# Optimization experiments

Measured on AMD Instinct MI355X. Metric: run time of the kernel, lower is better.

## Reference

```python
import jax, jax.numpy as jnp
import numpy as np
from jax import lax

B, T = 64, 2048
VOCAB, E, H = 50000, 256, 256
PADDING_TOKEN = 0

def setup_inputs() -> dict:
    key = jax.random.key(0)
    ks = jax.random.split(key, 7)
    batch_reviews = jax.random.randint(ks[0], (B, T), 0, VOCAB)
    batch_lengths = jax.random.randint(ks[1], (B,), 1, T + 1)  # valid lengths in [1, T]
    emb_table = jax.random.normal(ks[2], (VOCAB, E), dtype=jnp.float32)
    emb_table = emb_table.at[PADDING_TOKEN].set(0.0)
    s_ih = 1.0 / np.sqrt(H)
    W_ih = jax.random.uniform(ks[3], (H, E), minval=-s_ih, maxval=s_ih, dtype=jnp.float32)
    W_hh = jax.random.uniform(ks[4], (H, H), minval=-s_ih, maxval=s_ih, dtype=jnp.float32)
    s_c = 1.0 / np.sqrt(H)
    W_cls = jax.random.uniform(ks[5], (2, H), minval=-s_c, maxval=s_c, dtype=jnp.float32)
    b_cls = jax.random.uniform(ks[6], (2,), minval=-s_c, maxval=s_c, dtype=jnp.float32)
    return {"batch_reviews": batch_reviews, "batch_lengths": batch_lengths,
            "emb_table": emb_table, "W_ih": W_ih, "W_hh": W_hh,
            "W_cls": W_cls, "b_cls": b_cls}

def reference(batch_reviews, batch_lengths, emb_table, W_ih, W_hh, W_cls, b_cls):
    # padding_idx row contributes zero embedding
    table = emb_table.at[PADDING_TOKEN].set(0.0)
    data = table[batch_reviews]  # [B, T, E]
    # Precompute input projections for all steps in one GEMM: [B, T, H]
    x_proj = jnp.einsum('bte,he->bth', data, W_ih)
    h0 = jnp.zeros((data.shape[0], W_hh.shape[0]), dtype=data.dtype)

    def step(h, xp_t):  # xp_t: [B, H]
        h_new = jnp.tanh(xp_t + h @ W_hh.T)
        return h_new, h_new

    _, hs = lax.scan(step, h0, jnp.swapaxes(x_proj, 0, 1))  # hs: [T, B, H]
    hs = jnp.swapaxes(hs, 0, 1)  # [B, T, H]
    last = hs[jnp.arange(hs.shape[0]), batch_lengths - 1]  # [B, H]
    logits = last @ W_cls.T + b_cls  # [B, 2]
    return logits
```

## Files before the change

### kernel.cpp

```cpp
#include <hip/hip_runtime.h>
#include <hip/hip_bf16.h>

#define VOCAB 50000
#define EDIM 256
#define HDIM 256
#define BATCH 64
#define SEQ 2048

__global__ void k_transpose(const float* __restrict__ W, float* __restrict__ WT) {
    int idx = blockIdx.x * 256 + threadIdx.x;
    int e = idx >> 8;
    int i = idx & 255;
    WT[idx] = W[i * 256 + e];
}

__global__ __launch_bounds__(256) void k_project(const float* __restrict__ emb,
                                                 const float* __restrict__ WT,
                                                 float* __restrict__ P) {
    __shared__ float etile[32 * 256];
    const int v0 = blockIdx.x * 32;
    const int tid = threadIdx.x;

    #pragma unroll 4
    for (int k = 0; k < 32; ++k) {
        int v = v0 + k;
        etile[k * 256 + tid] = (v < VOCAB) ? emb[(size_t)v * 256 + tid] : 0.0f;
    }
    __syncthreads();

    float acc[32];
    #pragma unroll
    for (int k = 0; k < 32; ++k) acc[k] = 0.0f;

    for (int e0 = 0; e0 < 256; e0 += 4) {
        float w0 = WT[(size_t)(e0 + 0) * 256 + tid];
        float w1 = WT[(size_t)(e0 + 1) * 256 + tid];
        float w2 = WT[(size_t)(e0 + 2) * 256 + tid];
        float w3 = WT[(size_t)(e0 + 3) * 256 + tid];
        #pragma unroll
        for (int k = 0; k < 32; ++k) {
            float4 ev = *(const float4*)&etile[k * 256 + e0];
            acc[k] = fmaf(ev.x, w0, acc[k]);
            acc[k] = fmaf(ev.y, w1, acc[k]);
            acc[k] = fmaf(ev.z, w2, acc[k]);
            acc[k] = fmaf(ev.w, w3, acc[k]);
        }
    }
    #pragma unroll 4
    for (int k = 0; k < 32; ++k) {
        int v = v0 + k;
        if (v < VOCAB) P[(size_t)v * 256 + tid] = acc[k];
    }
}

__device__ __forceinline__ float tanh_fast(float x) {
    float ax = fabsf(x);
    float e  = __expf(-2.0f * ax);
    float r  = (1.0f - e) / (1.0f + e);
    return copysignf(r, x);
}

__global__ __launch_bounds__(512, 2) void k_rnn(const int* __restrict__ tokens,
                                                const int* __restrict__ lengths,
                                                const float* __restrict__ P,
                                                const float* __restrict__ Whh,
                                                const float* __restrict__ Wcls,
                                                const float* __restrict__ bcls,
                                                float* __restrict__ out) {
    __shared__ float h_lds[256];
    __shared__ float part[8][256];
    __shared__ int   tok_lds[SEQ];

    const int b   = blockIdx.x;
    const int tid = threadIdx.x;
    const int len = lengths[b];

    #pragma unroll
    for (int k = 0; k < 4; ++k)
        tok_lds[tid + k * 512] = tokens[b * SEQ + tid + k * 512];
    if (tid < 256) h_lds[tid] = 0.0f;

    const int rg = tid & 63;
    const int cg = tid >> 6;

    float4 w[4][8];
    #pragma unroll
    for (int j = 0; j < 4; ++j) {
        const float4* src = (const float4*)(Whh + (size_t)(4 * rg + j) * 256 + cg * 32);
        #pragma unroll
        for (int m = 0; m < 8; ++m) w[j][m] = src[m];
    }
    __syncthreads();

    float xp_cur = 0.0f, xp_next = 0.0f;
    if (tid < 256) xp_cur = P[(size_t)tok_lds[0] * 256 + tid];

    for (int t = 0; t < len; ++t) {
        if (tid < 256 && t + 1 < len) {
            int tn = tok_lds[t + 1];
            xp_next = P[(size_t)tn * 256 + tid];
        }

        const float4* hv = (const float4*)(h_lds + cg * 32);
        float a0 = 0.f, a1 = 0.f, a2 = 0.f, a3 = 0.f;
        #pragma unroll
        for (int m = 0; m < 8; ++m) {
            float4 h4 = hv[m];
            a0 = fmaf(w[0][m].x, h4.x, a0); a0 = fmaf(w[0][m].y, h4.y, a0);
            a0 = fmaf(w[0][m].z, h4.z, a0); a0 = fmaf(w[0][m].w, h4.w, a0);
            a1 = fmaf(w[1][m].x, h4.x, a1); a1 = fmaf(w[1][m].y, h4.y, a1);
            a1 = fmaf(w[1][m].z, h4.z, a1); a1 = fmaf(w[1][m].w, h4.w, a1);
            a2 = fmaf(w[2][m].x, h4.x, a2); a2 = fmaf(w[2][m].y, h4.y, a2);
            a2 = fmaf(w[2][m].z, h4.z, a2); a2 = fmaf(w[2][m].w, h4.w, a2);
            a3 = fmaf(w[3][m].x, h4.x, a3); a3 = fmaf(w[3][m].y, h4.y, a3);
            a3 = fmaf(w[3][m].z, h4.z, a3); a3 = fmaf(w[3][m].w, h4.w, a3);
        }
        *(float4*)&part[cg][4 * rg] = make_float4(a0, a1, a2, a3);
        __syncthreads();

        if (tid < 256) {
            float s0 = part[0][tid] + part[1][tid];
            float s1 = part[2][tid] + part[3][tid];
            float s2 = part[4][tid] + part[5][tid];
            float s3 = part[6][tid] + part[7][tid];
            float hn = tanh_fast(xp_cur + ((s0 + s1) + (s2 + s3)));
            h_lds[tid] = hn;
            xp_cur = xp_next;
        }
        __syncthreads();
    }

    if (tid < 128) {
        int c = tid >> 6, l = tid & 63;
        float sacc = 0.f;
        #pragma unroll
        for (int q = 0; q < 4; ++q)
            sacc += Wcls[c * 256 + q * 64 + l] * h_lds[q * 64 + l];
        #pragma unroll
        for (int off = 32; off > 0; off >>= 1)
            sacc += __shfl_down(sacc, off, 64);
        if (l == 0) out[b * 2 + c] = sacc + bcls[c];
    }
}

extern "C" void kernel_launch(void* const* d_in, const int* in_sizes, int n_in,
                              void* d_out, int out_size, void* d_ws, size_t ws_size,
                              hipStream_t stream) {
    const int*   reviews = (const int*)d_in[0];
    const int*   lengths = (const int*)d_in[1];
    const float* emb     = (const float*)d_in[2];
    const float* W_ih    = (const float*)d_in[3];
    const float* W_hh    = (const float*)d_in[4];
    const float* W_cls   = (const float*)d_in[5];
    const float* b_cls   = (const float*)d_in[6];
    float* out = (float*)d_out;

    float* WT = (float*)d_ws;
    float* P  = WT + 256 * 256;

    k_transpose<<<256, 256, 0, stream>>>(W_ih, WT);
    k_project<<<(VOCAB + 31) / 32, 256, 0, stream>>>(emb, WT, P);
    k_rnn<<<BATCH, 512, 0, stream>>>(reviews, lengths, P, W_hh, W_cls, b_cls, out);
}
```

Before: 1.518 ms.

## Reduce RNN matvec partials with wave shuffles and double-buffer hidden state

Each wave now owns 32 output rows, and the 8 column-group partial sums are reduced inside the wave with xor shuffles. This replaces the LDS partial-sum array and the second barrier per timestep. The hidden state is double-buffered in padded LDS (stride 36) to avoid bank conflicts, so only one __syncthreads per step remains. The cost is extra shuffle instructions, and only 8 lanes per wave compute tanh and write h.

```diff
diff --git a/kernel.cpp b/kernel.cpp
--- a/kernel.cpp
+++ b/kernel.cpp
@@ -6,6 +6,8 @@
 #define HDIM 256
 #define BATCH 64
 #define SEQ 2048
+
+#define GSTRIDE 36
 
 __global__ void k_transpose(const float* __restrict__ W, float* __restrict__ WT) {
     int idx = blockIdx.x * 256 + threadIdx.x;
@@ -67,8 +69,7 @@
                                                 const float* __restrict__ Wcls,
                                                 const float* __restrict__ bcls,
                                                 float* __restrict__ out) {
-    __shared__ float h_lds[256];
-    __shared__ float part[8][256];
+    __shared__ float hbuf[2][8 * GSTRIDE];
     __shared__ int   tok_lds[SEQ];
 
     const int b   = blockIdx.x;
@@ -78,68 +79,78 @@
     #pragma unroll
     for (int k = 0; k < 4; ++k)
         tok_lds[tid + k * 512] = tokens[b * SEQ + tid + k * 512];
-    if (tid < 256) h_lds[tid] = 0.0f;
+    if (tid < 8 * GSTRIDE) hbuf[0][tid] = 0.0f;
 
-    const int rg = tid & 63;
-    const int cg = tid >> 6;
+    const int w    = tid >> 6;
+    const int l    = tid & 63;
+    const int k8   = l & 7;
+    const int cgrp = l >> 3;
+    const int row0 = 32 * w + 4 * k8;
 
-    float4 w[4][8];
+    float4 wv[4][8];
     #pragma unroll
     for (int j = 0; j < 4; ++j) {
-        const float4* src = (const float4*)(Whh + (size_t)(4 * rg + j) * 256 + cg * 32);
+        const float4* src = (const float4*)(Whh + (size_t)(row0 + j) * 256 + 32 * cgrp);
         #pragma unroll
-        for (int m = 0; m < 8; ++m) w[j][m] = src[m];
+        for (int m = 0; m < 8; ++m) wv[j][m] = src[m];
     }
     __syncthreads();
 
-    float xp_cur = 0.0f, xp_next = 0.0f;
-    if (tid < 256) xp_cur = P[(size_t)tok_lds[0] * 256 + tid];
+    const bool fin = (l < 8);
+    float4 xp_cur = make_float4(0.f, 0.f, 0.f, 0.f), xp_next = xp_cur;
+    if (fin) xp_cur = *(const float4*)&P[(size_t)tok_lds[0] * 256 + row0];
 
     for (int t = 0; t < len; ++t) {
-        if (tid < 256 && t + 1 < len) {
-            int tn = tok_lds[t + 1];
-            xp_next = P[(size_t)tn * 256 + tid];
-        }
+        if (fin && t + 1 < len)
+            xp_next = *(const float4*)&P[(size_t)tok_lds[t + 1] * 256 + row0];
 
-        const float4* hv = (const float4*)(h_lds + cg * 32);
+        const float* hc = &hbuf[t & 1][cgrp * GSTRIDE];
         float a0 = 0.f, a1 = 0.f, a2 = 0.f, a3 = 0.f;
         #pragma unroll
         for (int m = 0; m < 8; ++m) {
-            float4 h4 = hv[m];
-            a0 = fmaf(w[0][m].x, h4.x, a0); a0 = fmaf(w[0][m].y, h4.y, a0);
-            a0 = fmaf(w[0][m].z, h4.z, a0); a0 = fmaf(w[0][m].w, h4.w, a0);
-            a1 = fmaf(w[1][m].x, h4.x, a1); a1 = fmaf(w[1][m].y, h4.y, a1);
-            a1 = fmaf(w[1][m].z, h4.z, a1); a1 = fmaf(w[1][m].w, h4.w, a1);
-            a2 = fmaf(w[2][m].x, h4.x, a2); a2 = fmaf(w[2][m].y, h4.y, a2);
-            a2 = fmaf(w[2][m].z, h4.z, a2); a2 = fmaf(w[2][m].w, h4.w, a2);
-            a3 = fmaf(w[3][m].x, h4.x, a3); a3 = fmaf(w[3][m].y, h4.y, a3);
-            a3 = fmaf(w[3][m].z, h4.z, a3); a3 = fmaf(w[3][m].w, h4.w, a3);
+            float4 h4 = *(const float4*)(hc + 4 * m);
+            a0 = fmaf(wv[0][m].x, h4.x, a0); a0 = fmaf(wv[0][m].y, h4.y, a0);
+            a0 = fmaf(wv[0][m].z, h4.z, a0); a0 = fmaf(wv[0][m].w, h4.w, a0);
+            a1 = fmaf(wv[1][m].x, h4.x, a1); a1 = fmaf(wv[1][m].y, h4.y, a1);
+            a1 = fmaf(wv[1][m].z, h4.z, a1); a1 = fmaf(wv[1][m].w, h4.w, a1);
+            a2 = fmaf(wv[2][m].x, h4.x, a2); a2 = fmaf(wv[2][m].y, h4.y, a2);
+            a2 = fmaf(wv[2][m].z, h4.z, a2); a2 = fmaf(wv[2][m].w, h4.w, a2);
+            a3 = fmaf(wv[3][m].x, h4.x, a3); a3 = fmaf(wv[3][m].y, h4.y, a3);
+            a3 = fmaf(wv[3][m].z, h4.z, a3); a3 = fmaf(wv[3][m].w, h4.w, a3);
         }
-        *(float4*)&part[cg][4 * rg] = make_float4(a0, a1, a2, a3);
-        __syncthreads();
 
-        if (tid < 256) {
-            float s0 = part[0][tid] + part[1][tid];
-            float s1 = part[2][tid] + part[3][tid];
-            float s2 = part[4][tid] + part[5][tid];
-            float s3 = part[6][tid] + part[7][tid];
-            float hn = tanh_fast(xp_cur + ((s0 + s1) + (s2 + s3)));
-            h_lds[tid] = hn;
+        a0 += __shfl_xor(a0, 8, 64);  a1 += __shfl_xor(a1, 8, 64);
+        a2 += __shfl_xor(a2, 8, 64);  a3 += __shfl_xor(a3, 8, 64);
+        a0 += __shfl_xor(a0, 16, 64); a1 += __shfl_xor(a1, 16, 64);
+        a2 += __shfl_xor(a2, 16, 64); a3 += __shfl_xor(a3, 16, 64);
+        a0 += __shfl_xor(a0, 32, 64); a1 += __shfl_xor(a1, 32, 64);
+        a2 += __shfl_xor(a2, 32, 64); a3 += __shfl_xor(a3, 32, 64);
+
+        if (fin) {
+            float4 hn;
+            hn.x = tanh_fast(xp_cur.x + a0);
+            hn.y = tanh_fast(xp_cur.y + a1);
+            hn.z = tanh_fast(xp_cur.z + a2);
+            hn.w = tanh_fast(xp_cur.w + a3);
+            *(float4*)&hbuf[(t + 1) & 1][w * GSTRIDE + 4 * l] = hn;
             xp_cur = xp_next;
         }
         __syncthreads();
     }
 
+    const float* hf = hbuf[len & 1];
     if (tid < 128) {
-        int c = tid >> 6, l = tid & 63;
+        int c = tid >> 6, l2 = tid & 63;
         float sacc = 0.f;
         #pragma unroll
-        for (int q = 0; q < 4; ++q)
-            sacc += Wcls[c * 256 + q * 64 + l] * h_lds[q * 64 + l];
+        for (int q = 0; q < 4; ++q) {
+            int idx = q * 64 + l2;
+            sacc += Wcls[c * 256 + idx] * hf[idx + ((idx >> 5) << 2)];
+        }
         #pragma unroll
         for (int off = 32; off > 0; off >>= 1)
             sacc += __shfl_down(sacc, off, 64);
-        if (l == 0) out[b * 2 + c] = sacc + bcls[c];
+        if (l2 == 0) out[b * 2 + c] = sacc + bcls[c];
     }
 }
 
```

After: 2.231 ms. 47.0% more time.
